# Kernel optimization log

Hardware: AMD Instinct MI355X
Metric: run time of the kernel (lower is better)

The kernel has to match this reference:

```python
import jax, jax.numpy as jnp
import numpy as np

SEQ, D_IN, D_OUT = 8192, 1024, 1024


def setup_inputs() -> dict:
    key = jax.random.key(0)
    kx, kq, kk, kv = jax.random.split(key, 4)
    # torch nn.Linear weights have shape (out_features, in_features)
    s = 1.0 / np.sqrt(D_IN)
    return {
        "x": jax.random.normal(kx, (SEQ, D_IN), dtype=jnp.float32),
        "Wq": jax.random.uniform(kq, (D_OUT, D_IN), dtype=jnp.float32, minval=-s, maxval=s),
        "Wk": jax.random.uniform(kk, (D_OUT, D_IN), dtype=jnp.float32, minval=-s, maxval=s),
        "Wv": jax.random.uniform(kv, (D_OUT, D_IN), dtype=jnp.float32, minval=-s, maxval=s),
    }


def reference(x, Wq, Wk, Wv):
    # Linear (no bias): y = x @ W.T
    q = x @ Wq.T          # [S, D_OUT]
    k = x @ Wk.T          # [S, D_OUT]
    v = x @ Wv.T          # [S, D_OUT]
    scale = 1.0 / jnp.sqrt(jnp.asarray(k.shape[-1], dtype=x.dtype))
    scores = (q @ k.T) * scale            # [S, S]
    weights = jax.nn.softmax(scores, axis=-1)
    return weights @ v                    # [S, D_OUT]
```

## Files before the change

### kernel.cpp

```cpp
#include <hip/hip_runtime.h>
#include <hip/hip_bf16.h>
#include <stdint.h>


#define SEQ 8192
#define DMODEL 1024
#define LOG2E 1.44269504088896340736f
#define GROUP_M 8

typedef __bf16 bf16_t;
typedef __bf16 bf16x8 __attribute__((ext_vector_type(8)));
typedef float f32x4 __attribute__((ext_vector_type(4)));

__global__ __launch_bounds__(256)
void convert_f32_bf16(const float* __restrict__ in, bf16_t* __restrict__ out, long n) {
    long i = ((long)blockIdx.x * 256 + threadIdx.x) * 4;
    if (i + 3 < n) {
        const float4 v = *(const float4*)(in + i);
        union { ushort4 u; bf16_t b[4]; } p;
        p.b[0] = (bf16_t)v.x; p.b[1] = (bf16_t)v.y;
        p.b[2] = (bf16_t)v.z; p.b[3] = (bf16_t)v.w;
        *(ushort4*)(out + i) = p.u;
    }
}

__global__ __launch_bounds__(256)
void add_f32(float* __restrict__ out, const float* __restrict__ part, long n) {
    long i = ((long)blockIdx.x * 256 + threadIdx.x) * 4;
    if (i + 3 < n) {
        float4 a = *(const float4*)(out + i);
        const float4 b = *(const float4*)(part + i);
        a.x += b.x; a.y += b.y; a.z += b.z; a.w += b.w;
        *(float4*)(out + i) = a;
    }
}

template <typename OutT>
__global__ __launch_bounds__(256, 3)
void gemm_nt(const bf16_t* __restrict__ A, const bf16_t* __restrict__ B,
             OutT* __restrict__ C0, OutT* __restrict__ C1,
             int M, int N, int Kps, int lda, int ldb, int ldc,
             long plane, int cshift, float alpha)
{
    __shared__ bf16_t As[128 * 64];
    __shared__ bf16_t Bs[128 * 64];

    const int tid  = threadIdx.x;
    const int wave = tid >> 6;
    const int lane = tid & 63;

    const int nbm = M >> 7, nbn = N >> 7;
    const int tiles = nbm * nbn;
    int bid = blockIdx.x;
    const int sid = bid / tiles;
    bid -= sid * tiles;
    const long kbase = (long)sid * Kps;
    OutT* __restrict__ C = sid ? C1 : C0;

    const int per_group = GROUP_M * nbn;
    const int gid   = bid / per_group;
    const int rem   = bid - gid * per_group;
    const int first = gid * GROUP_M;
    const int gsz   = min(nbm - first, GROUP_M);
    const int bm    = first + rem % gsz;
    const int bn    = rem / gsz;
    const long row0 = (long)bm * 128;
    const long col0 = (long)bn * 128;

    const int wm = (wave >> 1) * 64;
    const int wn = (wave & 1) * 64;
    const int lr = lane & 15;
    const int lq = lane >> 4;

    f32x4 acc[4][4] = {};

    for (int k0 = 0; k0 < Kps; k0 += 64) {
        #pragma unroll
        for (int i = 0; i < 4; ++i) {
            const int c = i * 256 + wave * 64 + lane;
            const int r = c >> 3, p = c & 7;
            const int l = (p + r) & 7;
            const bf16_t* ga = A + (row0 + r) * (long)lda + kbase + k0 + l * 8;
            const bf16_t* gb = B + (col0 + r) * (long)ldb + kbase + k0 + l * 8;
            __builtin_amdgcn_global_load_lds(
                (const __attribute__((address_space(1))) uint32_t*)ga,
                (__attribute__((address_space(3))) uint32_t*)(As + (long)c * 8),
                16, 0, 0);
            __builtin_amdgcn_global_load_lds(
                (const __attribute__((address_space(1))) uint32_t*)gb,
                (__attribute__((address_space(3))) uint32_t*)(Bs + (long)c * 8),
                16, 0, 0);
        }
        __syncthreads();

        #pragma unroll
        for (int t = 0; t < 2; ++t) {
            bf16x8 af[4], bfr[4];
            #pragma unroll
            for (int mi = 0; mi < 4; ++mi) {
                const int r = wm + mi * 16 + lr;
                const int p = (t * 4 + lq - r) & 7;
                af[mi] = *(const bf16x8*)(As + (long)r * 64 + p * 8);
            }
            #pragma unroll
            for (int ni = 0; ni < 4; ++ni) {
                const int r = wn + ni * 16 + lr;
                const int p = (t * 4 + lq - r) & 7;
                bfr[ni] = *(const bf16x8*)(Bs + (long)r * 64 + p * 8);
            }
            #pragma unroll
            for (int mi = 0; mi < 4; ++mi)
                #pragma unroll
                for (int ni = 0; ni < 4; ++ni)
                    acc[mi][ni] = __builtin_amdgcn_mfma_f32_16x16x32_bf16(
                        af[mi], bfr[ni], acc[mi][ni], 0, 0, 0);
        }
        __syncthreads();
    }

    OutT* __restrict__ Cb = C + (col0 >> cshift) * plane;
    const int ccol0 = (int)(col0 & (((long)1 << cshift) - 1));
    #pragma unroll
    for (int mi = 0; mi < 4; ++mi)
        #pragma unroll
        for (int ni = 0; ni < 4; ++ni)
            #pragma unroll
            for (int rg = 0; rg < 4; ++rg) {
                const long r = row0 + wm + mi * 16 + lq * 4 + rg;
                const int  c = ccol0 + wn + ni * 16 + lr;
                Cb[r * (long)ldc + c] = (OutT)(alpha * acc[mi][ni][rg]);
            }
}

__global__ __launch_bounds__(256)
void transpose_bf16(const bf16_t* __restrict__ in, bf16_t* __restrict__ out,
                    int R, int ldin, int ldout)
{
    __shared__ bf16_t tile[32][33];
    const int tx = threadIdx.x & 31;
    const int ty = threadIdx.x >> 5;
    const int c0 = blockIdx.x * 32;
    const int r0 = blockIdx.y * 32;
    #pragma unroll
    for (int j = 0; j < 32; j += 8)
        tile[ty + j][tx] = in[(long)(r0 + ty + j) * ldin + c0 + tx];
    __syncthreads();
    #pragma unroll
    for (int j = 0; j < 32; j += 8)
        out[(long)(c0 + ty + j) * ldout + r0 + tx] = tile[tx][ty + j];
}

__global__ __launch_bounds__(256)
void softmax_rows(bf16_t* __restrict__ S, int n)
{
    const long row = blockIdx.x;
    bf16_t* p = S + row * (long)n;
    const int tid = threadIdx.x;
    const int wave = tid >> 6, lane = tid & 63;
    __shared__ float red[4];

    float v[32];
    #pragma unroll
    for (int j = 0; j < 4; ++j) {
        bf16x8 x = *(const bf16x8*)(p + ((long)(j * 256 + tid)) * 8);
        #pragma unroll
        for (int e = 0; e < 8; ++e) v[j * 8 + e] = (float)x[e];
    }
    float m = -3.4e38f;
    #pragma unroll
    for (int i = 0; i < 32; ++i) m = fmaxf(m, v[i]);
    #pragma unroll
    for (int off = 32; off > 0; off >>= 1) m = fmaxf(m, __shfl_xor(m, off));
    if (lane == 0) red[wave] = m;
    __syncthreads();
    m = fmaxf(fmaxf(red[0], red[1]), fmaxf(red[2], red[3]));
    __syncthreads();

    float s = 0.f;
    #pragma unroll
    for (int i = 0; i < 32; ++i) { v[i] = exp2f((v[i] - m) * LOG2E); s += v[i]; }
    #pragma unroll
    for (int off = 32; off > 0; off >>= 1) s += __shfl_xor(s, off);
    if (lane == 0) red[wave] = s;
    __syncthreads();
    s = red[0] + red[1] + red[2] + red[3];
    const float inv = 1.f / s;

    #pragma unroll
    for (int j = 0; j < 4; ++j) {
        bf16x8 x;
        #pragma unroll
        for (int e = 0; e < 8; ++e) x[e] = (bf16_t)(v[j * 8 + e] * inv);
        *(bf16x8*)(p + ((long)(j * 256 + tid)) * 8) = x;
    }
}

extern "C" void kernel_launch(void* const* d_in, const int* in_sizes, int n_in,
                              void* d_out, int out_size, void* d_ws, size_t ws_size,
                              hipStream_t stream)
{
    const float* x  = (const float*)d_in[0];
    const float* Wq = (const float*)d_in[1];
    const float* Wk = (const float*)d_in[2];
    const float* Wv = (const float*)d_in[3];
    float* out = (float*)d_out;

    char* ws = (char*)d_ws;
    const long XN = (long)SEQ * DMODEL;
    const long WN = (long)DMODEL * DMODEL;
    const long SN = (long)SEQ * SEQ;

    bf16_t* xb   = (bf16_t*)ws;
    bf16_t* wcat = (bf16_t*)(ws + XN * 2);
    bf16_t* qb   = (bf16_t*)(ws + XN * 2 + WN * 6);
    bf16_t* kb   = qb + XN;
    bf16_t* vb   = qb + 2 * XN;
    bf16_t* Sb   = (bf16_t*)(ws + XN * 2 + WN * 6 + XN * 6);
    float*  pvp  = (float*)(ws + XN * 2 + WN * 6 + XN * 6 + SN * 2);
    bf16_t* vtb  = xb;

    const size_t need_split = (size_t)(XN * 2 + WN * 6 + XN * 6 + SN * 2) + XN * 4;
    const bool use_split = ws_size >= need_split;

    convert_f32_bf16<<<(int)(XN / 4 / 256), 256, 0, stream>>>(x,  xb, XN);
    convert_f32_bf16<<<(int)(WN / 4 / 256), 256, 0, stream>>>(Wq, wcat,          WN);
    convert_f32_bf16<<<(int)(WN / 4 / 256), 256, 0, stream>>>(Wk, wcat + WN,     WN);
    convert_f32_bf16<<<(int)(WN / 4 / 256), 256, 0, stream>>>(Wv, wcat + 2 * WN, WN);

    dim3 blk(256);
    gemm_nt<bf16_t><<<(SEQ / 128) * (3 * DMODEL / 128), blk, 0, stream>>>(
        xb, wcat, qb, qb, SEQ, 3 * DMODEL, DMODEL,
        DMODEL, DMODEL, DMODEL, XN, 10, 1.0f);

    transpose_bf16<<<dim3(DMODEL / 32, SEQ / 32), blk, 0, stream>>>(
        vb, vtb, SEQ, DMODEL, SEQ);

    gemm_nt<bf16_t><<<(SEQ / 128) * (SEQ / 128), blk, 0, stream>>>(
        qb, kb, Sb, Sb, SEQ, SEQ, DMODEL,
        DMODEL, DMODEL, SEQ, 0, 30, 0.03125f);

    softmax_rows<<<SEQ, blk, 0, stream>>>(Sb, SEQ);

    if (use_split) {
        gemm_nt<float><<<2 * (SEQ / 128) * (DMODEL / 128), blk, 0, stream>>>(
            Sb, vtb, out, pvp, SEQ, DMODEL, SEQ / 2,
            SEQ, SEQ, DMODEL, 0, 30, 1.0f);
        add_f32<<<(int)(XN / 4 / 256), 256, 0, stream>>>(out, pvp, XN);
    } else {
        gemm_nt<float><<<(SEQ / 128) * (DMODEL / 128), blk, 0, stream>>>(
            Sb, vtb, out, out, SEQ, DMODEL, SEQ,
            SEQ, SEQ, DMODEL, 0, 30, 1.0f);
    }
}
```

Baseline: 508.0 us.

## Fuse softmax exp and row sums into score GEMM epilogue, normalize in PV

Removes the standalone softmax kernel. The QK^T GEMM epilogue now writes exp2 of the scaled scores and atomically adds per-row sums into a zeroed buffer, and the PV GEMM epilogue divides by the row sum. This avoids a full read and write of the SEQxSEQ score matrix. It drops the row-max subtraction, so it relies on scores being small enough not to overflow exp, and in split mode each half is normalized before the partials are added.

```diff
diff --git a/kernel.cpp b/kernel.cpp
--- a/kernel.cpp
+++ b/kernel.cpp
@@ -35,10 +35,17 @@
     }
 }
 
-template <typename OutT>
+__global__ __launch_bounds__(256)
+void zero_f32(float* __restrict__ p, int n) {
+    int i = blockIdx.x * 256 + threadIdx.x;
+    if (i < n) p[i] = 0.0f;
+}
+
+template <typename OutT, int MODE>
 __global__ __launch_bounds__(256, 3)
 void gemm_nt(const bf16_t* __restrict__ A, const bf16_t* __restrict__ B,
              OutT* __restrict__ C0, OutT* __restrict__ C1,
+             float* __restrict__ lsum,
              int M, int N, int Kps, int lda, int ldb, int ldc,
              long plane, int cshift, float alpha)
 {
@@ -120,16 +127,52 @@
 
     OutT* __restrict__ Cb = C + (col0 >> cshift) * plane;
     const int ccol0 = (int)(col0 & (((long)1 << cshift) - 1));
-    #pragma unroll
-    for (int mi = 0; mi < 4; ++mi)
-        #pragma unroll
-        for (int ni = 0; ni < 4; ++ni)
+
+    if (MODE == 1) {
+        #pragma unroll
+        for (int mi = 0; mi < 4; ++mi)
             #pragma unroll
             for (int rg = 0; rg < 4; ++rg) {
                 const long r = row0 + wm + mi * 16 + lq * 4 + rg;
-                const int  c = ccol0 + wn + ni * 16 + lr;
-                Cb[r * (long)ldc + c] = (OutT)(alpha * acc[mi][ni][rg]);
-            }
+                float part = 0.f;
+                #pragma unroll
+                for (int ni = 0; ni < 4; ++ni) {
+                    const int c = ccol0 + wn + ni * 16 + lr;
+                    const float e = exp2f(alpha * acc[mi][ni][rg]);
+                    part += e;
+                    Cb[r * (long)ldc + c] = (OutT)e;
+                }
+                part += __shfl_xor(part, 1);
+                part += __shfl_xor(part, 2);
+                part += __shfl_xor(part, 4);
+                part += __shfl_xor(part, 8);
+                if (lr == 0) atomicAdd(&lsum[r], part);
+            }
+    } else if (MODE == 2) {
+        #pragma unroll
+        for (int mi = 0; mi < 4; ++mi)
+            #pragma unroll
+            for (int rg = 0; rg < 4; ++rg) {
+                const long r = row0 + wm + mi * 16 + lq * 4 + rg;
+                const float inv = 1.0f / lsum[r];
+                #pragma unroll
+                for (int ni = 0; ni < 4; ++ni) {
+                    const int c = ccol0 + wn + ni * 16 + lr;
+                    Cb[r * (long)ldc + c] = (OutT)(acc[mi][ni][rg] * inv);
+                }
+            }
+    } else {
+        #pragma unroll
+        for (int mi = 0; mi < 4; ++mi)
+            #pragma unroll
+            for (int ni = 0; ni < 4; ++ni)
+                #pragma unroll
+                for (int rg = 0; rg < 4; ++rg) {
+                    const long r = row0 + wm + mi * 16 + lq * 4 + rg;
+                    const int  c = ccol0 + wn + ni * 16 + lr;
+                    Cb[r * (long)ldc + c] = (OutT)(alpha * acc[mi][ni][rg]);
+                }
+    }
 }
 
 __global__ __launch_bounds__(256)
@@ -150,51 +193,6 @@
         out[(long)(c0 + ty + j) * ldout + r0 + tx] = tile[tx][ty + j];
 }
 
-__global__ __launch_bounds__(256)
-void softmax_rows(bf16_t* __restrict__ S, int n)
-{
-    const long row = blockIdx.x;
-    bf16_t* p = S + row * (long)n;
-    const int tid = threadIdx.x;
-    const int wave = tid >> 6, lane = tid & 63;
-    __shared__ float red[4];
-
-    float v[32];
-    #pragma unroll
-    for (int j = 0; j < 4; ++j) {
-        bf16x8 x = *(const bf16x8*)(p + ((long)(j * 256 + tid)) * 8);
-        #pragma unroll
-        for (int e = 0; e < 8; ++e) v[j * 8 + e] = (float)x[e];
-    }
-    float m = -3.4e38f;
-    #pragma unroll
-    for (int i = 0; i < 32; ++i) m = fmaxf(m, v[i]);
-    #pragma unroll
-    for (int off = 32; off > 0; off >>= 1) m = fmaxf(m, __shfl_xor(m, off));
-    if (lane == 0) red[wave] = m;
-    __syncthreads();
-    m = fmaxf(fmaxf(red[0], red[1]), fmaxf(red[2], red[3]));
-    __syncthreads();
-
-    float s = 0.f;
-    #pragma unroll
-    for (int i = 0; i < 32; ++i) { v[i] = exp2f((v[i] - m) * LOG2E); s += v[i]; }
-    #pragma unroll
-    for (int off = 32; off > 0; off >>= 1) s += __shfl_xor(s, off);
-    if (lane == 0) red[wave] = s;
-    __syncthreads();
-    s = red[0] + red[1] + red[2] + red[3];
-    const float inv = 1.f / s;
-
-    #pragma unroll
-    for (int j = 0; j < 4; ++j) {
-        bf16x8 x;
-        #pragma unroll
-        for (int e = 0; e < 8; ++e) x[e] = (bf16_t)(v[j * 8 + e] * inv);
-        *(bf16x8*)(p + ((long)(j * 256 + tid)) * 8) = x;
-    }
-}
-
 extern "C" void kernel_launch(void* const* d_in, const int* in_sizes, int n_in,
                               void* d_out, int out_size, void* d_ws, size_t ws_size,
                               hipStream_t stream)
@@ -217,38 +215,39 @@
     bf16_t* vb   = qb + 2 * XN;
     bf16_t* Sb   = (bf16_t*)(ws + XN * 2 + WN * 6 + XN * 6);
     float*  pvp  = (float*)(ws + XN * 2 + WN * 6 + XN * 6 + SN * 2);
+    float*  lsum = (float*)(ws + XN * 2 + WN * 6 + XN * 6 + SN * 2 + XN * 4);
     bf16_t* vtb  = xb;
 
-    const size_t need_split = (size_t)(XN * 2 + WN * 6 + XN * 6 + SN * 2) + XN * 4;
-    const bool use_split = ws_size >= need_split;
+    const size_t base_need = (size_t)(XN * 2 + WN * 6 + XN * 6 + SN * 2);
+    const bool use_split = ws_size >= base_need + XN * 4 + SEQ * 4;
+    if (!use_split) lsum = (float*)(ws + base_need);
 
     convert_f32_bf16<<<(int)(XN / 4 / 256), 256, 0, stream>>>(x,  xb, XN);
     convert_f32_bf16<<<(int)(WN / 4 / 256), 256, 0, stream>>>(Wq, wcat,          WN);
     convert_f32_bf16<<<(int)(WN / 4 / 256), 256, 0, stream>>>(Wk, wcat + WN,     WN);
     convert_f32_bf16<<<(int)(WN / 4 / 256), 256, 0, stream>>>(Wv, wcat + 2 * WN, WN);
+    zero_f32<<<SEQ / 256, 256, 0, stream>>>(lsum, SEQ);
 
     dim3 blk(256);
-    gemm_nt<bf16_t><<<(SEQ / 128) * (3 * DMODEL / 128), blk, 0, stream>>>(
-        xb, wcat, qb, qb, SEQ, 3 * DMODEL, DMODEL,
+    gemm_nt<bf16_t, 0><<<(SEQ / 128) * (3 * DMODEL / 128), blk, 0, stream>>>(
+        xb, wcat, qb, qb, nullptr, SEQ, 3 * DMODEL, DMODEL,
         DMODEL, DMODEL, DMODEL, XN, 10, 1.0f);
 
     transpose_bf16<<<dim3(DMODEL / 32, SEQ / 32), blk, 0, stream>>>(
         vb, vtb, SEQ, DMODEL, SEQ);
 
-    gemm_nt<bf16_t><<<(SEQ / 128) * (SEQ / 128), blk, 0, stream>>>(
-        qb, kb, Sb, Sb, SEQ, SEQ, DMODEL,
-        DMODEL, DMODEL, SEQ, 0, 30, 0.03125f);
-
-    softmax_rows<<<SEQ, blk, 0, stream>>>(Sb, SEQ);
+    gemm_nt<bf16_t, 1><<<(SEQ / 128) * (SEQ / 128), blk, 0, stream>>>(
+        qb, kb, Sb, Sb, lsum, SEQ, SEQ, DMODEL,
+        DMODEL, DMODEL, SEQ, 0, 30, 0.03125f * LOG2E);
 
     if (use_split) {
-        gemm_nt<float><<<2 * (SEQ / 128) * (DMODEL / 128), blk, 0, stream>>>(
-            Sb, vtb, out, pvp, SEQ, DMODEL, SEQ / 2,
+        gemm_nt<float, 2><<<2 * (SEQ / 128) * (DMODEL / 128), blk, 0, stream>>>(
+            Sb, vtb, out, pvp, lsum, SEQ, DMODEL, SEQ / 2,
             SEQ, SEQ, DMODEL, 0, 30, 1.0f);
         add_f32<<<(int)(XN / 4 / 256), 256, 0, stream>>>(out, pvp, XN);
     } else {
-        gemm_nt<float><<<(SEQ / 128) * (DMODEL / 128), blk, 0, stream>>>(
-            Sb, vtb, out, out, SEQ, DMODEL, SEQ,
+        gemm_nt<float, 2><<<(SEQ / 128) * (DMODEL / 128), blk, 0, stream>>>(
+            Sb, vtb, out, out, lsum, SEQ, DMODEL, SEQ,
             SEQ, SEQ, DMODEL, 0, 30, 1.0f);
     }
 }
```

Measured after the change: 504.2 us. Within noise of the previous version (-0.7%).
